# Optimization experiments

Measured on AMD Instinct MI355X. Metric: run time of the kernel, lower is better.

## Reference

```python
import jax, jax.numpy as jnp
import numpy as np

D_MODEL = 1024
NUM_HEADS = 16
HEAD_DIM = D_MODEL // NUM_HEADS


def setup_inputs() -> dict:
    key = jax.random.key(0)
    ks = jax.random.split(key, 9)
    s = 1.0 / np.sqrt(D_MODEL)
    return {
        "x": jax.random.normal(ks[0], (4, 2048, D_MODEL), dtype=jnp.float32),
        "Wq": jax.random.uniform(ks[1], (D_MODEL, D_MODEL), minval=-s, maxval=s, dtype=jnp.float32),
        "bq": jax.random.uniform(ks[2], (D_MODEL,), minval=-s, maxval=s, dtype=jnp.float32),
        "Wk": jax.random.uniform(ks[3], (D_MODEL, D_MODEL), minval=-s, maxval=s, dtype=jnp.float32),
        "bk": jax.random.uniform(ks[4], (D_MODEL,), minval=-s, maxval=s, dtype=jnp.float32),
        "Wv": jax.random.uniform(ks[5], (D_MODEL, D_MODEL), minval=-s, maxval=s, dtype=jnp.float32),
        "bv": jax.random.uniform(ks[6], (D_MODEL,), minval=-s, maxval=s, dtype=jnp.float32),
        "Wo": jax.random.uniform(ks[7], (D_MODEL, D_MODEL), minval=-s, maxval=s, dtype=jnp.float32),
        "bo": jax.random.uniform(ks[8], (D_MODEL,), minval=-s, maxval=s, dtype=jnp.float32),
    }


def reference(x, Wq, bq, Wk, bk, Wv, bv, Wo, bo):
    B, T, C = x.shape
    H, Dh = NUM_HEADS, HEAD_DIM
    # projections (nn.Linear applies x @ W^T + b)
    q = (x @ Wq.T + bq).reshape(B, T, H, Dh).transpose(0, 2, 1, 3)  # [B,H,T,Dh]
    k = (x @ Wk.T + bk).reshape(B, T, H, Dh).transpose(0, 2, 1, 3)
    v = (x @ Wv.T + bv).reshape(B, T, H, Dh).transpose(0, 2, 1, 3)
    scale = 1.0 / np.sqrt(Dh).astype(np.float32)
    att = jnp.einsum("bhqd,bhkd->bhqk", q, k) * scale  # [B,H,T,T]
    causal = jnp.tril(jnp.ones((T, T), dtype=bool))
    att = jnp.where(causal[None, None], att, -jnp.inf)
    att = jax.nn.softmax(att, axis=-1)
    # dropout is identity in eval mode
    out = jnp.einsum("bhqk,bhkd->bhqd", att, v)  # [B,H,T,Dh]
    out = out.transpose(0, 2, 1, 3).reshape(B, T, C)
    return out @ Wo.T + bo
```

## Files before the change

kernel.cpp:

```cpp
#include <hip/hip_runtime.h>
#include <stdint.h>

typedef __attribute__((ext_vector_type(8))) short short8;
typedef __attribute__((ext_vector_type(4))) short short4v;
typedef __attribute__((ext_vector_type(4))) float floatx4;

#define QSCALE 0.1803368801111f

__device__ __forceinline__ unsigned short f2bf(float f) {
  unsigned int u = __float_as_uint(f);
  unsigned int r = (u + 0x7FFFu + ((u >> 16) & 1u)) >> 16;
  return (unsigned short)r;
}

__device__ __forceinline__ unsigned int cvt_pk_bf16(float lo, float hi) {
  unsigned int r;
  asm("v_cvt_pk_bf16_f32 %0, %1, %2" : "=v"(r) : "v"(lo), "v"(hi));
  return r;
}

__device__ __forceinline__ void async_copy16(void* lds, const void* g) {
  __builtin_amdgcn_global_load_lds(
      (const __attribute__((address_space(1))) unsigned int*)g,
      (__attribute__((address_space(3))) unsigned int*)lds, 16, 0, 0);
}

__global__ __launch_bounds__(256) void f2b_kernel(const float* __restrict__ in,
                                                  unsigned short* __restrict__ out,
                                                  int n4) {
  int i = blockIdx.x * 256 + threadIdx.x;
  if (i >= n4) return;
  float4 v = ((const float4*)in)[i];
  short4v o;
  o[0] = (short)f2bf(v.x);
  o[1] = (short)f2bf(v.y);
  o[2] = (short)f2bf(v.z);
  o[3] = (short)f2bf(v.w);
  *(short4v*)(out + (long)i * 4) = o;
}

__device__ __forceinline__ void gemm128_mainloop(
    const unsigned short* __restrict__ A, const unsigned short* __restrict__ Bt,
    int K, long brow, long bcol, unsigned short* As, unsigned short* Bs,
    floatx4 acc[4][4]) {
  const int tid = threadIdx.x;
  const int wave = tid >> 6;
  const int lane = tid & 63;
  const int wr = wave >> 1, wc = wave & 1;
  const int lr = lane & 15, lg = lane >> 4;

  const unsigned short* ga = A + (brow + (tid >> 2)) * (long)K + (tid & 3) * 8;
  const unsigned short* gb = Bt + (bcol + (tid >> 2)) * (long)K + (tid & 3) * 8;
  unsigned short* lA = As + wave * 512;
  unsigned short* lB = Bs + wave * 512;
  const int a_off = (wr * 64 + lr) * 32 + lg * 8;
  const int b_off = (wc * 64 + lr) * 32 + lg * 8;

  for (int kt = 0; kt < K; kt += 32) {
    __syncthreads();
    async_copy16(lA, ga);
    async_copy16(lA + 2048, ga + (long)64 * K);
    async_copy16(lB, gb);
    async_copy16(lB + 2048, gb + (long)64 * K);
    ga += 32;
    gb += 32;
    __syncthreads();
    short8 af[4], bf[4];
#pragma unroll
    for (int i = 0; i < 4; ++i) {
      af[i] = *(const short8*)(As + a_off + i * 512);
      bf[i] = *(const short8*)(Bs + b_off + i * 512);
    }
#pragma unroll
    for (int i = 0; i < 4; ++i)
#pragma unroll
      for (int j = 0; j < 4; ++j)
        acc[i][j] = __builtin_amdgcn_mfma_f32_16x16x32_bf16(af[i], bf[j], acc[i][j], 0, 0, 0);
  }
}

__global__ __launch_bounds__(256) void qkv_gemm(
    const unsigned short* __restrict__ xb, const unsigned short* __restrict__ wqkv,
    const float* __restrict__ bq, const float* __restrict__ bk,
    const float* __restrict__ bv, unsigned short* __restrict__ q_out,
    unsigned short* __restrict__ k_out, unsigned short* __restrict__ vt_out) {
  __shared__ unsigned short As[128 * 32];
  __shared__ unsigned short Bs[128 * 32];
  floatx4 zero = {0.f, 0.f, 0.f, 0.f};
  floatx4 acc[4][4];
#pragma unroll
  for (int i = 0; i < 4; ++i)
#pragma unroll
    for (int j = 0; j < 4; ++j) acc[i][j] = zero;

  long brow = (long)blockIdx.x * 128;
  long bcol = (long)blockIdx.y * 128;
  gemm128_mainloop(xb, wqkv, 1024, brow, bcol, As, Bs, acc);

  const int wave = threadIdx.x >> 6, lane = threadIdx.x & 63;
  const int wr = wave >> 1, wc = wave & 1, lr = lane & 15, lg = lane >> 4;
  const int kind = (int)(bcol >> 10);
  const float* bias = (kind == 0) ? bq : (kind == 1 ? bk : bv);
#pragma unroll
  for (int i = 0; i < 4; ++i)
#pragma unroll
    for (int j = 0; j < 4; ++j)
#pragma unroll
      for (int r = 0; r < 4; ++r) {
        int m = (int)brow + wr * 64 + i * 16 + lg * 4 + r;
        int n = (int)bcol + wc * 64 + j * 16 + lr;
        int f = n & 1023;
        float v = acc[i][j][r] + bias[f];
        if (kind == 0) v *= QSCALE;
        unsigned short o = f2bf(v);
        int h = f >> 6, d = f & 63;
        int b = m >> 11, t = m & 2047;
        long bh = (long)(b * 16 + h);
        if (kind == 0)
          q_out[(bh * 2048 + t) * 64 + d] = o;
        else if (kind == 1)
          k_out[(bh * 2048 + t) * 64 + d] = o;
        else
          vt_out[(bh * 64 + d) * 2048 + t] = o;
      }
}

__global__ __launch_bounds__(256) void out_gemm(
    const unsigned short* __restrict__ ob, const unsigned short* __restrict__ wo,
    const float* __restrict__ bo, float* __restrict__ out) {
  __shared__ unsigned short As[128 * 32];
  __shared__ unsigned short Bs[128 * 32];
  floatx4 zero = {0.f, 0.f, 0.f, 0.f};
  floatx4 acc[4][4];
#pragma unroll
  for (int i = 0; i < 4; ++i)
#pragma unroll
    for (int j = 0; j < 4; ++j) acc[i][j] = zero;

  long brow = (long)blockIdx.x * 128;
  long bcol = (long)blockIdx.y * 128;
  gemm128_mainloop(ob, wo, 1024, brow, bcol, As, Bs, acc);

  const int wave = threadIdx.x >> 6, lane = threadIdx.x & 63;
  const int wr = wave >> 1, wc = wave & 1, lr = lane & 15, lg = lane >> 4;
#pragma unroll
  for (int i = 0; i < 4; ++i)
#pragma unroll
    for (int j = 0; j < 4; ++j)
#pragma unroll
      for (int r = 0; r < 4; ++r) {
        int m = (int)brow + wr * 64 + i * 16 + lg * 4 + r;
        int n = (int)bcol + wc * 64 + j * 16 + lr;
        out[(long)m * 1024 + n] = acc[i][j][r] + bo[n];
      }
}

__device__ __forceinline__ void stage_kv(char* __restrict__ Kb, char* __restrict__ Vb,
                                         const char* __restrict__ Kp,
                                         const char* __restrict__ Vt, int kv0,
                                         int tid) {
  const int wave = tid >> 6;
#pragma unroll
  for (int j = 0; j < 2; ++j) {
    int d = j * 256 + tid;
    int row = d >> 3, cc = d & 7;
    int gc = cc ^ (row & 7);
    const char* gk = Kp + (size_t)kv0 * 128 + row * 128 + gc * 16;
    async_copy16(Kb + (j * 256 + wave * 64) * 16, gk);
    const char* gv = Vt + (size_t)row * 4096 + (size_t)kv0 * 2 + gc * 16;
    async_copy16(Vb + (j * 256 + wave * 64) * 16, gv);
  }
}

__device__ __forceinline__ void attn_step(
    const char* __restrict__ Kb, const char* __restrict__ Vb,
    char* __restrict__ PTw, const short8& qf0, const short8& qf1,
    int kv0, int q0, int lr, int lg, bool diag,
    float& m_i, float& l_i, floatx4 accO[4]) {
  floatx4 zero = {0.f, 0.f, 0.f, 0.f};
  const int x7 = lr & 7;
  floatx4 s[4];
  __builtin_amdgcn_s_setprio(1);
#pragma unroll
  for (int nt = 0; nt < 4; ++nt) {
    const char* kr = Kb + (nt * 16 + lr) * 128;
    short8 kf0 = *(const short8*)(kr + ((lg ^ x7) * 16));
    short8 kf1 = *(const short8*)(kr + (((4 + lg) ^ x7) * 16));
    floatx4 a = zero;
    a = __builtin_amdgcn_mfma_f32_16x16x32_bf16(kf0, qf0, a, 0, 0, 0);
    a = __builtin_amdgcn_mfma_f32_16x16x32_bf16(kf1, qf1, a, 0, 0, 0);
    s[nt] = a;
  }
  __builtin_amdgcn_s_setprio(0);

  if (diag) {
    const int q = q0 + lr;
#pragma unroll
    for (int nt = 0; nt < 4; ++nt)
#pragma unroll
      for (int r = 0; r < 4; ++r) {
        int kvi = kv0 + nt * 16 + lg * 4 + r;
        if (kvi > q) s[nt][r] = -1e30f;
      }
  }
  float mnt[4];
#pragma unroll
  for (int nt = 0; nt < 4; ++nt)
    mnt[nt] = fmaxf(fmaxf(s[nt][0], s[nt][1]), fmaxf(s[nt][2], s[nt][3]));
  float pmax = fmaxf(fmaxf(mnt[0], mnt[1]), fmaxf(mnt[2], mnt[3]));

  if (__any(pmax > m_i + 11.5f)) {
    float mx = fmaxf(pmax, __shfl_xor(pmax, 16));
    mx = fmaxf(mx, __shfl_xor(mx, 32));
    float mnew = fmaxf(m_i, mx);
    float scl = exp2f(m_i - mnew);
    m_i = mnew;
    l_i *= scl;
#pragma unroll
    for (int r = 0; r < 4; ++r) {
      float so = __shfl(scl, lg * 4 + r);
#pragma unroll
      for (int dt = 0; dt < 4; ++dt) accO[dt][r] *= so;
    }
  }

#pragma unroll
  for (int nt = 0; nt < 4; ++nt) {
    float p0 = exp2f(s[nt][0] - m_i);
    float p1 = exp2f(s[nt][1] - m_i);
    float p2 = exp2f(s[nt][2] - m_i);
    float p3 = exp2f(s[nt][3] - m_i);
    l_i += (p0 + p1) + (p2 + p3);
    uint2 wv;
    wv.x = cvt_pk_bf16(p0, p1);
    wv.y = cvt_pk_bf16(p2, p3);
    *(uint2*)(PTw + lr * 128 + (((2 * nt + (lg >> 1)) ^ x7) * 16) + ((2 * lg) & 3) * 4) = wv;
  }

  __builtin_amdgcn_s_setprio(1);
#pragma unroll
  for (int kk = 0; kk < 2; ++kk) {
    short8 pf = *(const short8*)(PTw + lr * 128 + (((4 * kk + lg) ^ x7) * 16));
#pragma unroll
    for (int dt = 0; dt < 4; ++dt) {
      short8 vf = *(const short8*)(Vb + (dt * 16 + lr) * 128 + (((4 * kk + lg) ^ x7) * 16));
      accO[dt] = __builtin_amdgcn_mfma_f32_16x16x32_bf16(pf, vf, accO[dt], 0, 0, 0);
    }
  }
  __builtin_amdgcn_s_setprio(0);
}

__global__ __launch_bounds__(256, 4) void attn_fwd(
    const unsigned short* __restrict__ qb, const unsigned short* __restrict__ kb,
    const unsigned short* __restrict__ vtb, unsigned short* __restrict__ ob) {
  __shared__ __align__(16) char Kbuf[2][8192];
  __shared__ __align__(16) char Vbuf[2][8192];
  __shared__ __align__(16) char PTbuf[4][2048];

  const int F = blockIdx.y * 16 + blockIdx.x;
  const int c = F & 7, t = F >> 3;
  const int bh = c * 8 + (t >> 4);
  const int pr = t & 15;

  const int tid = threadIdx.x;
  const int wave = tid >> 6, lane = tid & 63;
  const int lr = lane & 15, lg = lane >> 4;
  const unsigned short* Q = qb + (long)bh * 2048 * 64;
  const char* Kp = (const char*)(kb + (long)bh * 2048 * 64);
  const char* Vt = (const char*)(vtb + (long)bh * 64 * 2048);
  const int b = bh >> 4, h = bh & 15;
  char* PTw = PTbuf[wave];

  floatx4 zero = {0.f, 0.f, 0.f, 0.f};

#pragma unroll 1
  for (int half = 0; half < 2; ++half) {
    const int qt = half ? (31 - pr) : pr;
    const int q0 = qt * 64 + wave * 16;
    const int nkv = qt + 1;

    short8 qf0 = *(const short8*)(Q + (q0 + lr) * 64 + lg * 8);
    short8 qf1 = *(const short8*)(Q + (q0 + lr) * 64 + 32 + lg * 8);

    floatx4 accO[4];
#pragma unroll
    for (int dt = 0; dt < 4; ++dt) accO[dt] = zero;
    float m_i = -1e30f, l_i = 0.f;

    stage_kv(Kbuf[0], Vbuf[0], Kp, Vt, 0, tid);
    __syncthreads();
#pragma unroll 1
    for (int kv = 0; kv < nkv; ++kv) {
      if (kv + 1 < nkv)
        stage_kv(Kbuf[(kv + 1) & 1], Vbuf[(kv + 1) & 1], Kp, Vt, (kv + 1) * 64, tid);
      attn_step(Kbuf[kv & 1], Vbuf[kv & 1], PTw, qf0, qf1, kv * 64, q0, lr, lg,
                kv == qt, m_i, l_i, accO);
      __syncthreads();
    }

    float lt = l_i + __shfl_xor(l_i, 16);
    lt += __shfl_xor(lt, 32);
    float linv = 1.f / lt;
#pragma unroll
    for (int r = 0; r < 4; ++r) {
      float io = __shfl(linv, lg * 4 + r);
      int tq = q0 + 4 * lg + r;
#pragma unroll
      for (int dt = 0; dt < 4; ++dt)
        ob[((long)b * 2048 + tq) * 1024 + h * 64 + dt * 16 + lr] =
            f2bf(accO[dt][r] * io);
    }
  }
}

extern "C" void kernel_launch(void* const* d_in, const int* in_sizes, int n_in,
                              void* d_out, int out_size, void* d_ws, size_t ws_size,
                              hipStream_t stream) {
  const float* x = (const float*)d_in[0];
  const float* bq = (const float*)d_in[2];
  const float* bk = (const float*)d_in[4];
  const float* bv = (const float*)d_in[6];
  const float* bo = (const float*)d_in[8];
  float* out = (float*)d_out;

  char* ws = (char*)d_ws;
  unsigned short* xb = (unsigned short*)(ws);
  unsigned short* wqkv = (unsigned short*)(ws + (16l << 20));
  unsigned short* wob = (unsigned short*)(ws + (22l << 20));
  unsigned short* qb = (unsigned short*)(ws + (24l << 20));
  unsigned short* kb = (unsigned short*)(ws + (40l << 20));
  unsigned short* vtb = (unsigned short*)(ws + (56l << 20));
  unsigned short* ob = (unsigned short*)(ws + (72l << 20));

  f2b_kernel<<<2097152 / 256, 256, 0, stream>>>(x, xb, 2097152);
  f2b_kernel<<<262144 / 256, 256, 0, stream>>>((const float*)d_in[1], wqkv, 262144);
  f2b_kernel<<<262144 / 256, 256, 0, stream>>>((const float*)d_in[3], wqkv + (1l << 20), 262144);
  f2b_kernel<<<262144 / 256, 256, 0, stream>>>((const float*)d_in[5], wqkv + (2l << 20), 262144);
  f2b_kernel<<<262144 / 256, 256, 0, stream>>>((const float*)d_in[7], wob, 262144);

  qkv_gemm<<<dim3(64, 24), 256, 0, stream>>>(xb, wqkv, bq, bk, bv, qb, kb, vtb);
  attn_fwd<<<dim3(16, 64), 256, 0, stream>>>(qb, kb, vtb, ob);
  out_gemm<<<dim3(64, 8), 256, 0, stream>>>(ob, wob, bo, out);
}
```

Measured before the change: 197.2 us.

## Replace QKV GEMM with 256x256-tile 8-wave double-buffered pipelined kernel

```diff
diff --git a/kernel.cpp b/kernel.cpp
--- a/kernel.cpp
+++ b/kernel.cpp
@@ -39,6 +39,148 @@
   *(short4v*)(out + (long)i * 4) = o;
 }
 
+__device__ __forceinline__ void stage_half_g(const char* __restrict__ gmat,
+                                             int grow0, int kbyte,
+                                             char* __restrict__ lds_base, int tid) {
+  const int wv = tid >> 6;
+#pragma unroll
+  for (int j = 0; j < 2; ++j) {
+    int s = j * 512 + tid;
+    int row = s >> 3, cph = s & 7;
+    int cl = cph ^ (row & 7);
+    async_copy16(lds_base + (j * 512 + wv * 64) * 16,
+                 gmat + (long)(grow0 + row) * 2048 + kbyte + cl * 16);
+  }
+}
+
+template <int QM, int QN>
+__device__ __forceinline__ void gemm_phase(const char* __restrict__ Asl,
+                                           const char* __restrict__ Bsl, int buf,
+                                           int wm, int wn, int lr, int lg,
+                                           floatx4 acc[2][2][4][2]) {
+  const char* Ab = Asl + (buf * 2 + QM) * 16384;
+  const char* Bb = Bsl + (buf * 2 + QN) * 16384;
+  short8 av[4][2], bv[2][2];
+#pragma unroll
+  for (int m = 0; m < 4; ++m) {
+    int R = wm * 64 + m * 16 + lr;
+#pragma unroll
+    for (int ks = 0; ks < 2; ++ks)
+      av[m][ks] = *(const short8*)(Ab + R * 128 + (((ks * 4 + lg) ^ (R & 7)) * 16));
+  }
+#pragma unroll
+  for (int n = 0; n < 2; ++n) {
+    int R = wn * 32 + n * 16 + lr;
+#pragma unroll
+    for (int ks = 0; ks < 2; ++ks)
+      bv[n][ks] = *(const short8*)(Bb + R * 128 + (((ks * 4 + lg) ^ (R & 7)) * 16));
+  }
+  __builtin_amdgcn_s_setprio(1);
+#pragma unroll
+  for (int m = 0; m < 4; ++m)
+#pragma unroll
+    for (int n = 0; n < 2; ++n)
+#pragma unroll
+      for (int ks = 0; ks < 2; ++ks)
+        acc[QM][QN][m][n] = __builtin_amdgcn_mfma_f32_16x16x32_bf16(
+            av[m][ks], bv[n][ks], acc[QM][QN][m][n], 0, 0, 0);
+  __builtin_amdgcn_s_setprio(0);
+}
+
+#define PH_SYNC(WAIT)                                    \
+  do {                                                   \
+    if (WAIT) asm volatile("s_waitcnt vmcnt(4)" ::: "memory"); \
+    __builtin_amdgcn_s_barrier();                        \
+    __builtin_amdgcn_sched_barrier(0);                   \
+  } while (0)
+
+__global__ __launch_bounds__(512, 1) void qkv_gemm8(
+    const unsigned short* __restrict__ xb, const unsigned short* __restrict__ wqkv,
+    const float* __restrict__ bq, const float* __restrict__ bk,
+    const float* __restrict__ bv, unsigned short* __restrict__ q_out,
+    unsigned short* __restrict__ k_out, unsigned short* __restrict__ vt_out) {
+  __shared__ __align__(16) char Lds[131072];
+  char* Asl = Lds;
+  char* Bsl = Lds + 65536;
+  const char* Ag = (const char*)xb;
+  const char* Bg = (const char*)wqkv;
+
+  const int bid = blockIdx.x;
+  const int gid = (bid & 7) * 48 + (bid >> 3);
+  const int brow = (gid % 32) * 256;
+  const int bcol = (gid / 32) * 256;
+
+  const int tid = threadIdx.x;
+  const int wv = tid >> 6, lane = tid & 63;
+  const int wm = wv >> 2, wn = wv & 3;
+  const int lr = lane & 15, lg = lane >> 4;
+
+  floatx4 acc[2][2][4][2];
+#pragma unroll
+  for (int a = 0; a < 2; ++a)
+#pragma unroll
+    for (int b = 0; b < 2; ++b)
+#pragma unroll
+      for (int m = 0; m < 4; ++m)
+#pragma unroll
+        for (int n = 0; n < 2; ++n) acc[a][b][m][n] = floatx4{0.f, 0.f, 0.f, 0.f};
+
+  stage_half_g(Ag, brow, 0, Asl + 0 * 16384, tid);
+  stage_half_g(Bg, bcol, 0, Bsl + 0 * 16384, tid);
+  stage_half_g(Bg, bcol + 128, 0, Bsl + 1 * 16384, tid);
+  stage_half_g(Ag, brow + 128, 0, Asl + 1 * 16384, tid);
+
+  int buf = 0;
+#pragma unroll 1
+  for (int t = 0; t < 16; ++t) {
+    const int nt = (t + 1) & 15;
+    const int kb = nt * 128;
+    const int nb = buf ^ 1;
+    PH_SYNC(1);
+    stage_half_g(Ag, brow, kb, Asl + (nb * 2 + 0) * 16384, tid);
+    gemm_phase<0, 0>(Asl, Bsl, buf, wm, wn, lr, lg, acc);
+    PH_SYNC(1);
+    stage_half_g(Bg, bcol, kb, Bsl + (nb * 2 + 0) * 16384, tid);
+    gemm_phase<0, 1>(Asl, Bsl, buf, wm, wn, lr, lg, acc);
+    PH_SYNC(1);
+    stage_half_g(Bg, bcol + 128, kb, Bsl + (nb * 2 + 1) * 16384, tid);
+    gemm_phase<1, 0>(Asl, Bsl, buf, wm, wn, lr, lg, acc);
+    PH_SYNC(0);
+    stage_half_g(Ag, brow + 128, kb, Asl + (nb * 2 + 1) * 16384, tid);
+    gemm_phase<1, 1>(Asl, Bsl, buf, wm, wn, lr, lg, acc);
+    buf = nb;
+  }
+
+  const int kind = bcol >> 10;
+  const float* bias = (kind == 0) ? bq : (kind == 1 ? bk : bv);
+#pragma unroll
+  for (int qm = 0; qm < 2; ++qm)
+#pragma unroll
+    for (int qn = 0; qn < 2; ++qn)
+#pragma unroll
+      for (int m = 0; m < 4; ++m)
+#pragma unroll
+        for (int n = 0; n < 2; ++n)
+#pragma unroll
+          for (int r = 0; r < 4; ++r) {
+            int gm = brow + qm * 128 + wm * 64 + m * 16 + lg * 4 + r;
+            int gn = bcol + qn * 128 + wn * 32 + n * 16 + lr;
+            int f = gn & 1023;
+            float v = acc[qm][qn][m][n][r] + bias[f];
+            if (kind == 0) v *= QSCALE;
+            unsigned short o = f2bf(v);
+            int h = f >> 6, d = f & 63;
+            int bb = gm >> 11, tt = gm & 2047;
+            long bh = (long)(bb * 16 + h);
+            if (kind == 0)
+              q_out[(bh * 2048 + tt) * 64 + d] = o;
+            else if (kind == 1)
+              k_out[(bh * 2048 + tt) * 64 + d] = o;
+            else
+              vt_out[(bh * 64 + d) * 2048 + tt] = o;
+          }
+}
+
 __device__ __forceinline__ void gemm128_mainloop(
     const unsigned short* __restrict__ A, const unsigned short* __restrict__ Bt,
     int K, long brow, long bcol, unsigned short* As, unsigned short* Bs,
@@ -79,52 +221,6 @@
   }
 }
 
-__global__ __launch_bounds__(256) void qkv_gemm(
-    const unsigned short* __restrict__ xb, const unsigned short* __restrict__ wqkv,
-    const float* __restrict__ bq, const float* __restrict__ bk,
-    const float* __restrict__ bv, unsigned short* __restrict__ q_out,
-    unsigned short* __restrict__ k_out, unsigned short* __restrict__ vt_out) {
-  __shared__ unsigned short As[128 * 32];
-  __shared__ unsigned short Bs[128 * 32];
-  floatx4 zero = {0.f, 0.f, 0.f, 0.f};
-  floatx4 acc[4][4];
-#pragma unroll
-  for (int i = 0; i < 4; ++i)
-#pragma unroll
-    for (int j = 0; j < 4; ++j) acc[i][j] = zero;
-
-  long brow = (long)blockIdx.x * 128;
-  long bcol = (long)blockIdx.y * 128;
-  gemm128_mainloop(xb, wqkv, 1024, brow, bcol, As, Bs, acc);
-
-  const int wave = threadIdx.x >> 6, lane = threadIdx.x & 63;
-  const int wr = wave >> 1, wc = wave & 1, lr = lane & 15, lg = lane >> 4;
-  const int kind = (int)(bcol >> 10);
-  const float* bias = (kind == 0) ? bq : (kind == 1 ? bk : bv);
-#pragma unroll
-  for (int i = 0; i < 4; ++i)
-#pragma unroll
-    for (int j = 0; j < 4; ++j)
-#pragma unroll
-      for (int r = 0; r < 4; ++r) {
-        int m = (int)brow + wr * 64 + i * 16 + lg * 4 + r;
-        int n = (int)bcol + wc * 64 + j * 16 + lr;
-        int f = n & 1023;
-        float v = acc[i][j][r] + bias[f];
-        if (kind == 0) v *= QSCALE;
-        unsigned short o = f2bf(v);
-        int h = f >> 6, d = f & 63;
-        int b = m >> 11, t = m & 2047;
-        long bh = (long)(b * 16 + h);
-        if (kind == 0)
-          q_out[(bh * 2048 + t) * 64 + d] = o;
-        else if (kind == 1)
-          k_out[(bh * 2048 + t) * 64 + d] = o;
-        else
-          vt_out[(bh * 64 + d) * 2048 + t] = o;
-      }
-}
-
 __global__ __launch_bounds__(256) void out_gemm(
     const unsigned short* __restrict__ ob, const unsigned short* __restrict__ wo,
     const float* __restrict__ bo, float* __restrict__ out) {
@@ -338,7 +434,7 @@
   f2b_kernel<<<262144 / 256, 256, 0, stream>>>((const float*)d_in[5], wqkv + (2l << 20), 262144);
   f2b_kernel<<<262144 / 256, 256, 0, stream>>>((const float*)d_in[7], wob, 262144);
 
-  qkv_gemm<<<dim3(64, 24), 256, 0, stream>>>(xb, wqkv, bq, bk, bv, qb, kb, vtb);
+  qkv_gemm8<<<384, 512, 0, stream>>>(xb, wqkv, bq, bk, bv, qb, kb, vtb);
   attn_fwd<<<dim3(16, 64), 256, 0, stream>>>(qb, kb, vtb, ob);
   out_gemm<<<dim3(64, 8), 256, 0, stream>>>(ob, wob, bo, out);
 }
```

Measured after the change: 232.4 us. 1.18x slower.

## Double per-wave query rows in attention and merge weight conversion launches

Applied to the files above, without the earlier changes.

```diff
diff --git a/kernel.cpp b/kernel.cpp
--- a/kernel.cpp
+++ b/kernel.cpp
@@ -30,6 +30,24 @@
                                                   int n4) {
   int i = blockIdx.x * 256 + threadIdx.x;
   if (i >= n4) return;
+  float4 v = ((const float4*)in)[i];
+  short4v o;
+  o[0] = (short)f2bf(v.x);
+  o[1] = (short)f2bf(v.y);
+  o[2] = (short)f2bf(v.z);
+  o[3] = (short)f2bf(v.w);
+  *(short4v*)(out + (long)i * 4) = o;
+}
+
+__global__ __launch_bounds__(256) void f2b4_kernel(
+    const float* __restrict__ w0, const float* __restrict__ w1,
+    const float* __restrict__ w2, const float* __restrict__ w3,
+    unsigned short* __restrict__ o0, unsigned short* __restrict__ o1,
+    unsigned short* __restrict__ o2, unsigned short* __restrict__ o3) {
+  int which = blockIdx.x >> 10;
+  const float* in = (which == 0) ? w0 : (which == 1) ? w1 : (which == 2) ? w2 : w3;
+  unsigned short* out = (which == 0) ? o0 : (which == 1) ? o1 : (which == 2) ? o2 : o3;
+  int i = (blockIdx.x & 1023) * 256 + threadIdx.x;
   float4 v = ((const float4*)in)[i];
   short4v o;
   o[0] = (short)f2bf(v.x);
@@ -174,93 +192,112 @@
 
 __device__ __forceinline__ void attn_step(
     const char* __restrict__ Kb, const char* __restrict__ Vb,
-    char* __restrict__ PTw, const short8& qf0, const short8& qf1,
+    char* __restrict__ PTw, const short8 (&qf)[2][2],
     int kv0, int q0, int lr, int lg, bool diag,
-    float& m_i, float& l_i, floatx4 accO[4]) {
+    float (&m_i)[2], float (&l_i)[2], floatx4 (&accO)[2][4]) {
   floatx4 zero = {0.f, 0.f, 0.f, 0.f};
   const int x7 = lr & 7;
-  floatx4 s[4];
+  floatx4 s[2][4];
   __builtin_amdgcn_s_setprio(1);
 #pragma unroll
   for (int nt = 0; nt < 4; ++nt) {
     const char* kr = Kb + (nt * 16 + lr) * 128;
     short8 kf0 = *(const short8*)(kr + ((lg ^ x7) * 16));
     short8 kf1 = *(const short8*)(kr + (((4 + lg) ^ x7) * 16));
-    floatx4 a = zero;
-    a = __builtin_amdgcn_mfma_f32_16x16x32_bf16(kf0, qf0, a, 0, 0, 0);
-    a = __builtin_amdgcn_mfma_f32_16x16x32_bf16(kf1, qf1, a, 0, 0, 0);
-    s[nt] = a;
+#pragma unroll
+    for (int qa = 0; qa < 2; ++qa) {
+      floatx4 a = zero;
+      a = __builtin_amdgcn_mfma_f32_16x16x32_bf16(kf0, qf[qa][0], a, 0, 0, 0);
+      a = __builtin_amdgcn_mfma_f32_16x16x32_bf16(kf1, qf[qa][1], a, 0, 0, 0);
+      s[qa][nt] = a;
+    }
   }
   __builtin_amdgcn_s_setprio(0);
 
   if (diag) {
-    const int q = q0 + lr;
-#pragma unroll
-    for (int nt = 0; nt < 4; ++nt)
+#pragma unroll
+    for (int qa = 0; qa < 2; ++qa) {
+      const int q = q0 + qa * 16 + lr;
+#pragma unroll
+      for (int nt = 0; nt < 4; ++nt)
+#pragma unroll
+        for (int r = 0; r < 4; ++r) {
+          int kvi = kv0 + nt * 16 + lg * 4 + r;
+          if (kvi > q) s[qa][nt][r] = -1e30f;
+        }
+    }
+  }
+
+  float pmax[2];
+#pragma unroll
+  for (int qa = 0; qa < 2; ++qa) {
+    float m0 = fmaxf(fmaxf(s[qa][0][0], s[qa][0][1]), fmaxf(s[qa][0][2], s[qa][0][3]));
+    float m1 = fmaxf(fmaxf(s[qa][1][0], s[qa][1][1]), fmaxf(s[qa][1][2], s[qa][1][3]));
+    float m2 = fmaxf(fmaxf(s[qa][2][0], s[qa][2][1]), fmaxf(s[qa][2][2], s[qa][2][3]));
+    float m3 = fmaxf(fmaxf(s[qa][3][0], s[qa][3][1]), fmaxf(s[qa][3][2], s[qa][3][3]));
+    pmax[qa] = fmaxf(fmaxf(m0, m1), fmaxf(m2, m3));
+  }
+
+  float g = fmaxf(pmax[0] - m_i[0], pmax[1] - m_i[1]);
+  if (__any(g > 11.5f)) {
+#pragma unroll
+    for (int qa = 0; qa < 2; ++qa) {
+      float mx = fmaxf(pmax[qa], __shfl_xor(pmax[qa], 16));
+      mx = fmaxf(mx, __shfl_xor(mx, 32));
+      float mnew = fmaxf(m_i[qa], mx);
+      float scl = exp2f(m_i[qa] - mnew);
+      m_i[qa] = mnew;
+      l_i[qa] *= scl;
 #pragma unroll
       for (int r = 0; r < 4; ++r) {
-        int kvi = kv0 + nt * 16 + lg * 4 + r;
-        if (kvi > q) s[nt][r] = -1e30f;
+        float so = __shfl(scl, lg * 4 + r);
+#pragma unroll
+        for (int dt = 0; dt < 4; ++dt) accO[qa][dt][r] *= so;
       }
-  }
-  float mnt[4];
-#pragma unroll
-  for (int nt = 0; nt < 4; ++nt)
-    mnt[nt] = fmaxf(fmaxf(s[nt][0], s[nt][1]), fmaxf(s[nt][2], s[nt][3]));
-  float pmax = fmaxf(fmaxf(mnt[0], mnt[1]), fmaxf(mnt[2], mnt[3]));
-
-  if (__any(pmax > m_i + 11.5f)) {
-    float mx = fmaxf(pmax, __shfl_xor(pmax, 16));
-    mx = fmaxf(mx, __shfl_xor(mx, 32));
-    float mnew = fmaxf(m_i, mx);
-    float scl = exp2f(m_i - mnew);
-    m_i = mnew;
-    l_i *= scl;
-#pragma unroll
-    for (int r = 0; r < 4; ++r) {
-      float so = __shfl(scl, lg * 4 + r);
-#pragma unroll
-      for (int dt = 0; dt < 4; ++dt) accO[dt][r] *= so;
-    }
-  }
-
-#pragma unroll
-  for (int nt = 0; nt < 4; ++nt) {
-    float p0 = exp2f(s[nt][0] - m_i);
-    float p1 = exp2f(s[nt][1] - m_i);
-    float p2 = exp2f(s[nt][2] - m_i);
-    float p3 = exp2f(s[nt][3] - m_i);
-    l_i += (p0 + p1) + (p2 + p3);
-    uint2 wv;
-    wv.x = cvt_pk_bf16(p0, p1);
-    wv.y = cvt_pk_bf16(p2, p3);
-    *(uint2*)(PTw + lr * 128 + (((2 * nt + (lg >> 1)) ^ x7) * 16) + ((2 * lg) & 3) * 4) = wv;
+    }
+  }
+
+#pragma unroll
+  for (int qa = 0; qa < 2; ++qa) {
+    char* prow = PTw + (qa * 16 + lr) * 128;
+#pragma unroll
+    for (int nt = 0; nt < 4; ++nt) {
+      float p0 = exp2f(s[qa][nt][0] - m_i[qa]);
+      float p1 = exp2f(s[qa][nt][1] - m_i[qa]);
+      float p2 = exp2f(s[qa][nt][2] - m_i[qa]);
+      float p3 = exp2f(s[qa][nt][3] - m_i[qa]);
+      l_i[qa] += (p0 + p1) + (p2 + p3);
+      uint2 wv;
+      wv.x = cvt_pk_bf16(p0, p1);
+      wv.y = cvt_pk_bf16(p2, p3);
+      *(uint2*)(prow + (((2 * nt + (lg >> 1)) ^ x7) * 16) + ((2 * lg) & 3) * 4) = wv;
+    }
   }
 
   __builtin_amdgcn_s_setprio(1);
 #pragma unroll
   for (int kk = 0; kk < 2; ++kk) {
-    short8 pf = *(const short8*)(PTw + lr * 128 + (((4 * kk + lg) ^ x7) * 16));
+    short8 pf0 = *(const short8*)(PTw + lr * 128 + (((4 * kk + lg) ^ x7) * 16));
+    short8 pf1 = *(const short8*)(PTw + (16 + lr) * 128 + (((4 * kk + lg) ^ x7) * 16));
 #pragma unroll
     for (int dt = 0; dt < 4; ++dt) {
       short8 vf = *(const short8*)(Vb + (dt * 16 + lr) * 128 + (((4 * kk + lg) ^ x7) * 16));
-      accO[dt] = __builtin_amdgcn_mfma_f32_16x16x32_bf16(pf, vf, accO[dt], 0, 0, 0);
+      accO[0][dt] = __builtin_amdgcn_mfma_f32_16x16x32_bf16(pf0, vf, accO[0][dt], 0, 0, 0);
+      accO[1][dt] = __builtin_amdgcn_mfma_f32_16x16x32_bf16(pf1, vf, accO[1][dt], 0, 0, 0);
     }
   }
   __builtin_amdgcn_s_setprio(0);
 }
 
-__global__ __launch_bounds__(256, 4) void attn_fwd(
+__global__ __launch_bounds__(256, 2) void attn_fwd(
     const unsigned short* __restrict__ qb, const unsigned short* __restrict__ kb,
     const unsigned short* __restrict__ vtb, unsigned short* __restrict__ ob) {
   __shared__ __align__(16) char Kbuf[2][8192];
   __shared__ __align__(16) char Vbuf[2][8192];
-  __shared__ __align__(16) char PTbuf[4][2048];
-
-  const int F = blockIdx.y * 16 + blockIdx.x;
-  const int c = F & 7, t = F >> 3;
-  const int bh = c * 8 + (t >> 4);
-  const int pr = t & 15;
+  __shared__ __align__(16) char PTbuf[4][4096];
+
+  const int bh = blockIdx.x * 8 + (blockIdx.y & 7);
+  const int pr = blockIdx.y >> 3;
 
   const int tid = threadIdx.x;
   const int wave = tid >> 6, lane = tid & 63;
@@ -275,17 +312,24 @@
 
 #pragma unroll 1
   for (int half = 0; half < 2; ++half) {
-    const int qt = half ? (31 - pr) : pr;
-    const int q0 = qt * 64 + wave * 16;
-    const int nkv = qt + 1;
-
-    short8 qf0 = *(const short8*)(Q + (q0 + lr) * 64 + lg * 8);
-    short8 qf1 = *(const short8*)(Q + (q0 + lr) * 64 + 32 + lg * 8);
-
-    floatx4 accO[4];
-#pragma unroll
-    for (int dt = 0; dt < 4; ++dt) accO[dt] = zero;
-    float m_i = -1e30f, l_i = 0.f;
+    const int qt = half ? (15 - pr) : pr;
+    const int q0 = qt * 128 + wave * 32;
+    const int nkv = 2 * qt + 2;
+
+    short8 qf[2][2];
+#pragma unroll
+    for (int qa = 0; qa < 2; ++qa)
+#pragma unroll
+      for (int kk = 0; kk < 2; ++kk)
+        qf[qa][kk] = *(const short8*)(Q + (q0 + qa * 16 + lr) * 64 + kk * 32 + lg * 8);
+
+    floatx4 accO[2][4];
+#pragma unroll
+    for (int qa = 0; qa < 2; ++qa)
+#pragma unroll
+      for (int dt = 0; dt < 4; ++dt) accO[qa][dt] = zero;
+    float m_i[2] = {-1e30f, -1e30f};
+    float l_i[2] = {0.f, 0.f};
 
     stage_kv(Kbuf[0], Vbuf[0], Kp, Vt, 0, tid);
     __syncthreads();
@@ -293,22 +337,25 @@
     for (int kv = 0; kv < nkv; ++kv) {
       if (kv + 1 < nkv)
         stage_kv(Kbuf[(kv + 1) & 1], Vbuf[(kv + 1) & 1], Kp, Vt, (kv + 1) * 64, tid);
-      attn_step(Kbuf[kv & 1], Vbuf[kv & 1], PTw, qf0, qf1, kv * 64, q0, lr, lg,
-                kv == qt, m_i, l_i, accO);
+      attn_step(Kbuf[kv & 1], Vbuf[kv & 1], PTw, qf, kv * 64, q0, lr, lg,
+                kv >= 2 * qt, m_i, l_i, accO);
       __syncthreads();
     }
 
-    float lt = l_i + __shfl_xor(l_i, 16);
-    lt += __shfl_xor(lt, 32);
-    float linv = 1.f / lt;
-#pragma unroll
-    for (int r = 0; r < 4; ++r) {
-      float io = __shfl(linv, lg * 4 + r);
-      int tq = q0 + 4 * lg + r;
-#pragma unroll
-      for (int dt = 0; dt < 4; ++dt)
-        ob[((long)b * 2048 + tq) * 1024 + h * 64 + dt * 16 + lr] =
-            f2bf(accO[dt][r] * io);
+#pragma unroll
+    for (int qa = 0; qa < 2; ++qa) {
+      float lt = l_i[qa] + __shfl_xor(l_i[qa], 16);
+      lt += __shfl_xor(lt, 32);
+      float linv = 1.f / lt;
+#pragma unroll
+      for (int r = 0; r < 4; ++r) {
+        float io = __shfl(linv, lg * 4 + r);
+        int tq = q0 + qa * 16 + 4 * lg + r;
+#pragma unroll
+        for (int dt = 0; dt < 4; ++dt)
+          ob[((long)b * 2048 + tq) * 1024 + h * 64 + dt * 16 + lr] =
+              f2bf(accO[qa][dt][r] * io);
+      }
     }
   }
 }
@@ -333,12 +380,11 @@
   unsigned short* ob = (unsigned short*)(ws + (72l << 20));
 
   f2b_kernel<<<2097152 / 256, 256, 0, stream>>>(x, xb, 2097152);
-  f2b_kernel<<<262144 / 256, 256, 0, stream>>>((const float*)d_in[1], wqkv, 262144);
-  f2b_kernel<<<262144 / 256, 256, 0, stream>>>((const float*)d_in[3], wqkv + (1l << 20), 262144);
-  f2b_kernel<<<262144 / 256, 256, 0, stream>>>((const float*)d_in[5], wqkv + (2l << 20), 262144);
-  f2b_kernel<<<262144 / 256, 256, 0, stream>>>((const float*)d_in[7], wob, 262144);
+  f2b4_kernel<<<4096, 256, 0, stream>>>(
+      (const float*)d_in[1], (const float*)d_in[3], (const float*)d_in[5],
+      (const float*)d_in[7], wqkv, wqkv + (1l << 20), wqkv + (2l << 20), wob);
 
   qkv_gemm<<<dim3(64, 24), 256, 0, stream>>>(xb, wqkv, bq, bk, bv, qb, kb, vtb);
-  attn_fwd<<<dim3(16, 64), 256, 0, stream>>>(qb, kb, vtb, ob);
+  attn_fwd<<<dim3(8, 64), 256, 0, stream>>>(qb, kb, vtb, ob);
   out_gemm<<<dim3(64, 8), 256, 0, stream>>>(ob, wob, bo, out);
 }
```

After: 195.3 us. No clear change (-1.0%).
